# Kernel tuning notes

Measured on AMD Instinct MI355X. Metric: run time of the kernel, lower is better.

Reference implementation:

```python
import jax, jax.numpy as jnp
import numpy as np
import math

T = 2048; HID = 2048; H = 16; KV = 8; G = H // KV; D = 128
GH = 128; BS = 64; NB = T // BS
EPS = 1e-6; RATIO = 0.2; SCALE = 1.0 / math.sqrt(D)


def _rope_tables(length, dim, theta=1000000.0):
    inv = 1.0 / (theta ** (np.arange(0, dim, 2, dtype=np.float32) / dim))
    f = np.outer(np.arange(length, dtype=np.float32), inv)
    emb = np.concatenate([f, f], axis=-1)
    return jnp.asarray(np.cos(emb)), jnp.asarray(np.sin(emb))


def _rot_half(x):
    d = x.shape[-1] // 2
    return jnp.concatenate([-x[..., d:], x[..., :d]], axis=-1)


def _apply_rope(x, cos, sin):
    # x: [T, nH, D], cos/sin: [T, D] broadcast over head dim
    return x * cos[:, None, :] + _rot_half(x) * sin[:, None, :]


def _rmsnorm(x, w, eps=EPS):
    xf = x.astype(jnp.float32)
    v = jnp.mean(xf * xf, axis=-1, keepdims=True)
    return (w * (xf * jax.lax.rsqrt(v + eps))).astype(x.dtype)


def setup_inputs() -> dict:
    key = jax.random.key(0)
    ks = jax.random.split(key, 8)
    s = 0.02
    hidden_states = jax.random.normal(ks[0], (T, HID), jnp.float32)
    Wq = jax.random.normal(ks[1], (HID, H * D), jnp.float32) * s
    Wk = jax.random.normal(ks[2], (HID, KV * D), jnp.float32) * s
    Wv = jax.random.normal(ks[3], (HID, KV * D), jnp.float32) * s
    Wo = jax.random.normal(ks[4], (H * D, HID), jnp.float32) * s
    q_norm_w = jnp.ones((D,), jnp.float32)
    k_norm_w = jnp.ones((D,), jnp.float32)
    gate_wq = jax.random.normal(ks[5], (D, GH), jnp.float32) * s
    gate_wk = jax.random.normal(ks[6], (D, GH), jnp.float32) * s
    cos, sin = _rope_tables(T, D)
    cos_gq, sin_gq = _rope_tables(T, GH)
    cos_blk, sin_blk = _rope_tables(NB, GH)
    # causal block mask: query t may attend to key block j iff j <= t // BS
    block_attention_mask = (jnp.arange(T)[:, None] // BS) >= jnp.arange(NB)[None, :]
    return dict(hidden_states=hidden_states, Wq=Wq, Wk=Wk, Wv=Wv, Wo=Wo,
                q_norm_w=q_norm_w, k_norm_w=k_norm_w, gate_wq=gate_wq, gate_wk=gate_wk,
                cos=cos, sin=sin, cos_gq=cos_gq, sin_gq=sin_gq,
                cos_blk=cos_blk, sin_blk=sin_blk,
                block_attention_mask=block_attention_mask)


def reference(hidden_states, Wq, Wk, Wv, Wo, q_norm_w, k_norm_w, gate_wq, gate_wk,
              cos, sin, cos_gq, sin_gq, cos_blk, sin_blk, block_attention_mask):
    q = (hidden_states @ Wq).reshape(T, H, D)
    k = (hidden_states @ Wk).reshape(T, KV, D)
    v = (hidden_states @ Wv).reshape(T, KV, D)
    q = _rmsnorm(q, q_norm_w)
    k = _rmsnorm(k, k_norm_w)

    # ---- gate network on un-roped q/k: q-head avg-pool to KV heads, k avg-pool per block ----
    q_pool = q.reshape(T, KV, G, D).mean(axis=2)            # [T, KV, D]
    gq = _apply_rope(q_pool @ gate_wq, cos_gq, sin_gq)      # [T, KV, GH]
    k_blk = k.reshape(NB, BS, KV, D).mean(axis=1)           # [NB, KV, D]
    gk = _apply_rope(k_blk @ gate_wk, cos_blk, sin_blk)     # [NB, KV, GH]
    gate_scores = jnp.einsum('tkg,nkg->ktn', gq, gk) / math.sqrt(GH)  # [KV, T, NB]
    predict_mask = jnp.where(block_attention_mask[None], gate_scores, -1e9)

    # ---- main attention (RoPE + GQA causal softmax attention) ----
    qr = _apply_rope(q, cos, sin)
    kr = _apply_rope(k, cos, sin)
    kr_rep = jnp.repeat(kr, G, axis=1)                      # [T, H, D]
    v_rep = jnp.repeat(v, G, axis=1)
    logits = jnp.einsum('thd,shd->hts', qr, kr_rep) * SCALE  # [H, T, T]
    causal = jnp.tril(jnp.ones((T, T), bool))
    logits = jnp.where(causal[None], logits, -jnp.inf)
    probs = jax.nn.softmax(logits, axis=-1)
    attn_output = jnp.einsum('hts,shd->thd', probs, v_rep).reshape(T, H * D) @ Wo

    # ---- pooled ground-truth block mask: attention mass per key block ----
    pooled = probs.reshape(H, T, NB, BS).sum(axis=-1)        # [H, T, NB]
    gt = pooled.reshape(KV, G, T, NB).max(axis=1)            # max_pool3d over head groups -> [KV,T,NB]
    gt = jnp.where(block_attention_mask[None], gt, 0.0)
    gt = gt / (gt.sum(axis=-1, keepdims=True) + 1e-9)

    # ---- KLDiv gate loss on the tail slice (bsz = 1) ----
    start = int(T * RATIO)
    tgt = gt[:, start:, :]                                   # [KV, L, NB]
    logp = jax.nn.log_softmax(predict_mask[:, start:, :], axis=-1)
    safe_t = jnp.where(tgt > 0, tgt, 1.0)
    kl = jnp.where(tgt > 0, tgt * (jnp.log(safe_t) - logp), 0.0)
    gate_loss = kl.reshape(KV, -1).mean(axis=-1).sum()       # KLDivLoss(reduction='mean') per kv head, summed, /bsz(=1)
    return attn_output, gate_loss
```

## Files before the change

### kernel.cpp

```cpp
#include <hip/hip_runtime.h>

#define T_ 2048
#define HID_ 2048
#define H_ 16
#define KV_ 8
#define G_ 2
#define D_ 128
#define GH_ 128
#define BS_ 64
#define NB_ 32
#define START_ 409
#define TG0_ 384
#define SCALE_ 0.08838834764831845f
#define MFIX_ 8.0f

typedef __attribute__((ext_vector_type(8))) short short8_t;
typedef __attribute__((ext_vector_type(4))) float float4_t;
typedef __attribute__((ext_vector_type(8))) unsigned short ushort8_t;
typedef __attribute__((ext_vector_type(4))) unsigned short ushort4_t;

__device__ __forceinline__ float wave_sum(float v) {
#pragma unroll
  for (int o = 32; o > 0; o >>= 1) v += __shfl_xor(v, o, 64);
  return v;
}
__device__ __forceinline__ unsigned short f2bf(float x) {
  unsigned int u = __float_as_uint(x);
  unsigned int r = (u + 0x7fffu + ((u >> 16) & 1u)) >> 16;
  return (unsigned short)r;
}

__device__ __forceinline__ void gload16(const void* g, void* l) {
  __builtin_amdgcn_global_load_lds((const __attribute__((address_space(1))) unsigned int*)g,
                                   (__attribute__((address_space(3))) unsigned int*)l, 16, 0, 0);
}

__device__ __forceinline__ void castT_dev(const float* __restrict__ in,
                                          unsigned short* __restrict__ out, int K, int N,
                                          int ldin, int bx, int by,
                                          unsigned short (*tile)[72], int tid) {
  int k0 = by * 64, n0 = bx * 64;
  int tx = tid & 63, ty4 = tid >> 6;
#pragma unroll
  for (int i = 0; i < 16; ++i) {
    int ky = ty4 * 16 + i;
    tile[tx][ky] = f2bf(in[(size_t)(k0 + ky) * ldin + n0 + tx]);
  }
  __syncthreads();
#pragma unroll
  for (int i = 0; i < 16; ++i) {
    int ny = ty4 * 16 + i;
    out[(size_t)(n0 + ny) * K + k0 + tx] = tile[ny][tx];
  }
}

__global__ __launch_bounds__(256) void prep_cast(const float* __restrict__ hs,
                                                 const float* __restrict__ Wq,
                                                 const float* __restrict__ Wk,
                                                 const float* __restrict__ Wv,
                                                 const float* __restrict__ Wo,
                                                 const float* __restrict__ gwq,
                                                 const float* __restrict__ gwk,
                                                 unsigned short* __restrict__ hsb,
                                                 unsigned short* __restrict__ WqkvT,
                                                 unsigned short* __restrict__ WoT,
                                                 unsigned short* __restrict__ gwqT,
                                                 unsigned short* __restrict__ gwkT) {
  __shared__ unsigned short tile[64][72];
  int id = blockIdx.x, tid = threadIdx.x;
  if (id < 4096) {
    int i = id * 256 + tid;
    float4 v = ((const float4*)hs)[i];
    ushort4_t o = {f2bf(v.x), f2bf(v.y), f2bf(v.z), f2bf(v.w)};
    *(ushort4_t*)(hsb + (size_t)i * 4) = o;
  } else if (id < 5120) {
    int t = id - 4096;
    castT_dev(Wq, WqkvT, 2048, 2048, 2048, t & 31, t >> 5, tile, tid);
  } else if (id < 5632) {
    int t = id - 5120;
    castT_dev(Wk, WqkvT + (size_t)2048 * 2048, 2048, 1024, 1024, t & 15, t >> 4, tile, tid);
  } else if (id < 6144) {
    int t = id - 5632;
    castT_dev(Wv, WqkvT + (size_t)3072 * 2048, 2048, 1024, 1024, t & 15, t >> 4, tile, tid);
  } else if (id < 7168) {
    int t = id - 6144;
    castT_dev(Wo, WoT, 2048, 2048, 2048, t & 31, t >> 5, tile, tid);
  } else if (id < 7172) {
    int t = id - 7168;
    castT_dev(gwq, gwqT, 128, 128, 128, t & 1, t >> 1, tile, tid);
  } else {
    int t = id - 7172;
    castT_dev(gwk, gwkT, 128, 128, 128, t & 1, t >> 1, tile, tid);
  }
}

__device__ __forceinline__ void gemm_body(const unsigned short* __restrict__ A,
                                          const unsigned short* __restrict__ Bt,
                                          float* __restrict__ C,
                                          int M, int N, int K, int ldc, int bx, int by,
                                          unsigned short* As, unsigned short* Bs) {
  int tid = threadIdx.x;
  int wid = tid >> 6, lane = tid & 63;
  int quad = lane >> 4, l16 = lane & 15;
  int wm = wid & 1, wn = wid >> 1;
  int m0 = by * 128, n0 = bx * 128;
  const unsigned short* gA[4];
  const unsigned short* gB[4];
#pragma unroll
  for (int it = 0; it < 4; ++it) {
    int line = wid * 32 + it * 8 + (lane >> 3);
    int chunk = (lane & 7) ^ (line & 7);
    gA[it] = A + (size_t)(m0 + line) * K + chunk * 8;
    gB[it] = Bt + (size_t)(n0 + line) * K + chunk * 8;
  }
  float4_t acc[4][4];
#pragma unroll
  for (int i = 0; i < 4; ++i)
#pragma unroll
    for (int j = 0; j < 4; ++j) acc[i][j] = (float4_t){0.f, 0.f, 0.f, 0.f};
  int nk = K >> 6;
#pragma unroll
  for (int it = 0; it < 4; ++it) {
    gload16(gA[it], As + (wid * 32 + it * 8) * 64);
    gload16(gB[it], Bs + (wid * 32 + it * 8) * 64);
  }
  for (int t = 0; t < nk; ++t) {
    __syncthreads();
    if (t + 1 < nk) {
      int bo = ((t + 1) & 1) * 8192;
#pragma unroll
      for (int it = 0; it < 4; ++it) {
        gload16(gA[it] + (t + 1) * 64, As + bo + (wid * 32 + it * 8) * 64);
        gload16(gB[it] + (t + 1) * 64, Bs + bo + (wid * 32 + it * 8) * 64);
      }
    }
    const unsigned short* Asc = As + (t & 1) * 8192;
    const unsigned short* Bsc = Bs + (t & 1) * 8192;
    short8_t a[2][4], b[2][4];
#pragma unroll
    for (int ks = 0; ks < 2; ++ks) {
      int sw = ((ks * 4 + quad) ^ (l16 & 7)) * 8;
#pragma unroll
      for (int i = 0; i < 4; ++i) {
        a[ks][i] = *(const short8_t*)&Asc[(wm * 64 + i * 16 + l16) * 64 + sw];
        b[ks][i] = *(const short8_t*)&Bsc[(wn * 64 + i * 16 + l16) * 64 + sw];
      }
    }
#pragma unroll
    for (int ks = 0; ks < 2; ++ks)
#pragma unroll
      for (int i = 0; i < 4; ++i)
#pragma unroll
        for (int j = 0; j < 4; ++j)
          acc[i][j] = __builtin_amdgcn_mfma_f32_16x16x32_bf16(a[ks][i], b[ks][j], acc[i][j], 0, 0, 0);
  }
#pragma unroll
  for (int i = 0; i < 4; ++i)
#pragma unroll
    for (int j = 0; j < 4; ++j)
#pragma unroll
      for (int reg = 0; reg < 4; ++reg)
        C[(size_t)(m0 + wm * 64 + i * 16 + quad * 4 + reg) * ldc + n0 + wn * 64 + j * 16 + l16] =
            acc[i][j][reg];
}

__global__ __launch_bounds__(256) void gemm_bf16_v3(const unsigned short* __restrict__ A,
                                                    const unsigned short* __restrict__ Bt,
                                                    float* __restrict__ C,
                                                    int M, int N, int K, int ldc) {
  __shared__ unsigned short As[2 * 128 * 64];
  __shared__ unsigned short Bs[2 * 128 * 64];
  int lin = blockIdx.y * gridDim.x + blockIdx.x;
  int nwg = gridDim.x * gridDim.y;
  int q = nwg >> 3;
  int v = (lin & 7) * q + (lin >> 3);
  int bx = v % gridDim.x, by = v / gridDim.x;
  gemm_body(A, Bt, C, M, N, K, ldc, bx, by, As, Bs);
}

__global__ __launch_bounds__(256) void gemm_gates(const unsigned short* __restrict__ Aq,
                                                  const unsigned short* __restrict__ Bq,
                                                  float* __restrict__ Cq,
                                                  const unsigned short* __restrict__ Ak,
                                                  const unsigned short* __restrict__ Bk,
                                                  float* __restrict__ Ck) {
  __shared__ unsigned short As[2 * 128 * 64];
  __shared__ unsigned short Bs[2 * 128 * 64];
  int y = blockIdx.y;
  if (y < 104)
    gemm_body(Aq, Bq, Cq, 13312, 128, 128, 128, 0, y, As, Bs);
  else
    gemm_body(Ak, Bk, Ck, 256, 128, 128, 128, 0, y - 104, As, Bs);
}

__global__ __launch_bounds__(128) void norm_rope_fused(const float* __restrict__ qkvf,
                                                       const float* __restrict__ qw,
                                                       const float* __restrict__ kw,
                                                       const float* __restrict__ cosT,
                                                       const float* __restrict__ sinT,
                                                       unsigned short* __restrict__ qbf,
                                                       unsigned short* __restrict__ qpool_bf,
                                                       unsigned short* __restrict__ kbf,
                                                       float* __restrict__ knorm) {
  int t = blockIdx.x, d = threadIdx.x;
  int kv = blockIdx.y;
  float cv = cosT[t * D_ + d], sv = sinT[t * D_ + d];
  {
    size_t i0 = (size_t)t * 4096 + (kv * G_) * D_ + d;
    float x0 = qkvf[i0], x1 = qkvf[i0 + D_];
    __shared__ float sred[2][2];
    float s0 = wave_sum(x0 * x0), s1 = wave_sum(x1 * x1);
    if ((d & 63) == 0) { sred[0][d >> 6] = s0; sred[1][d >> 6] = s1; }
    __syncthreads();
    float wv = qw[d];
    float n0 = x0 * rsqrtf((sred[0][0] + sred[0][1]) * (1.f / D_) + 1e-6f) * wv;
    float n1 = x1 * rsqrtf((sred[1][0] + sred[1][1]) * (1.f / D_) + 1e-6f) * wv;
    if (t >= TG0_) qpool_bf[((size_t)(t - TG0_) * KV_ + kv) * D_ + d] = f2bf(0.5f * (n0 + n1));
    __shared__ float sh[2][D_];
    sh[0][d] = n0; sh[1][d] = n1;
    __syncthreads();
    float r0 = (d < 64) ? -sh[0][d + 64] : sh[0][d - 64];
    float r1 = (d < 64) ? -sh[1][d + 64] : sh[1][d - 64];
    qbf[((size_t)(t * H_) + kv * G_) * D_ + d] = f2bf(n0 * cv + r0 * sv);
    qbf[((size_t)(t * H_) + kv * G_ + 1) * D_ + d] = f2bf(n1 * cv + r1 * sv);
  }
  __syncthreads();
  {
    float x = qkvf[(size_t)t * 4096 + 2048 + kv * D_ + d];
    __shared__ float sredk[2];
    float s0 = wave_sum(x * x);
    if ((d & 63) == 0) sredk[d >> 6] = s0;
    __syncthreads();
    float nk = x * rsqrtf((sredk[0] + sredk[1]) * (1.f / D_) + 1e-6f) * kw[d];
    knorm[(size_t)(t * KV_ + kv) * D_ + d] = nk;
    __shared__ float shk[D_];
    shk[d] = nk;
    __syncthreads();
    float rot = (d < 64) ? -shk[d + 64] : shk[d - 64];
    kbf[(size_t)(t * KV_ + kv) * D_ + d] = f2bf(nk * cv + rot * sv);
  }
}

__global__ __launch_bounds__(256) void castT_kblk(const float* __restrict__ qkvf,
                                                  unsigned short* __restrict__ vt,
                                                  const float* __restrict__ knorm,
                                                  unsigned short* __restrict__ kblk_bf) {
  __shared__ unsigned short tile[64][72];
  int id = blockIdx.x, tid = threadIdx.x;
  if (id < 512) {
    castT_dev(qkvf + 3072, vt, T_, 1024, 4096, id & 15, id >> 4, tile, tid);
  } else {
    int task = (id - 512) * 2 + (tid >> 7);
    int n = task >> 3, kv = task & 7, d = tid & 127;
    float s = 0.f;
    for (int i = 0; i < BS_; ++i) s += knorm[((size_t)(n * BS_ + i) * KV_ + kv) * D_ + d];
    kblk_bf[(size_t)(n * KV_ + kv) * D_ + d] = f2bf(s * (1.f / BS_));
  }
}

__global__ __launch_bounds__(128) void rope_g_fused(float* __restrict__ gq, float* __restrict__ gk,
                                                    const float* __restrict__ cosG,
                                                    const float* __restrict__ sinG,
                                                    const float* __restrict__ cosB,
                                                    const float* __restrict__ sinB) {
  int r = blockIdx.x, kvh = blockIdx.y, d = threadIdx.x;
  float* x;
  size_t base;
  float c_, s_;
  if (r < NB_) {
    x = gk;
    base = (size_t)(r * KV_ + kvh) * GH_;
    c_ = cosB[r * GH_ + d]; s_ = sinB[r * GH_ + d];
  } else {
    int rr = r - NB_;
    x = gq;
    base = (size_t)(rr * KV_ + kvh) * GH_;
    c_ = cosG[(size_t)(TG0_ + rr) * GH_ + d]; s_ = sinG[(size_t)(TG0_ + rr) * GH_ + d];
  }
  __shared__ float sh[GH_];
  sh[d] = x[base + d];
  __syncthreads();
  float rot = (d < 64) ? -sh[d + 64] : sh[d - 64];
  x[base + d] = sh[d] * c_ + rot * s_;
}

__global__ __launch_bounds__(256, 2) void attn_mfma(const unsigned short* __restrict__ qbf,
                                                    const unsigned short* __restrict__ kbf,
                                                    const unsigned short* __restrict__ vt,
                                                    float* __restrict__ pooled,
                                                    float* __restrict__ o_acc,
                                                    float* __restrict__ l_acc) {
  int kv = blockIdx.x;
  int yy = blockIdx.y;
  int tile, c_lo, c_hi;
  if (yy < 32) { tile = yy;      c_lo = 0;                c_hi = (tile + 2) >> 1; }
  else         { tile = 63 - yy; c_lo = (tile + 2) >> 1;  c_hi = tile + 1; }
  int t0 = tile * 64;
  int tid = threadIdx.x;
  int wid = tid >> 6, lane = tid & 63;
  int quad = lane >> 4, l16 = lane & 15;
  __shared__ unsigned short Ks[2][64 * 128];
  __shared__ unsigned short Vs[2][128 * 64];
  __shared__ unsigned short Ps[8][16 * 64];

  const unsigned short* kbase[4];
  const unsigned short* vbase[4];
#pragma unroll
  for (int it = 0; it < 4; ++it) {
    int seg = wid * 4 + it;
    int krow = seg * 4 + (lane >> 4);
    int kchk = lane & 15;
    kbase[it] = kbf + ((size_t)krow * KV_ + kv) * D_ + ((kchk ^ (krow & 7)) << 3);
    int vrow = seg * 8 + (lane >> 3);
    int vchk = lane & 7;
    vbase[it] = vt + (size_t)(kv * 128 + vrow) * T_ + ((vchk ^ (vrow & 7)) << 3);
  }

  int tq = t0 + wid * 16 + l16;
  short8_t qf[2][4];
#pragma unroll
  for (int hh = 0; hh < 2; ++hh)
#pragma unroll
    for (int kb = 0; kb < 4; ++kb)
      qf[hh][kb] = *(const short8_t*)&qbf[((size_t)tq * H_ + kv * G_ + hh) * D_ + kb * 32 + quad * 8];

  const short one_bf = (short)0x3F80;
  short8_t ones = {one_bf, one_bf, one_bf, one_bf, one_bf, one_bf, one_bf, one_bf};

  int tbase = t0 + wid * 16 + quad * 4;
  float l_[2][4] = {};
  float pacc[2][2][4] = {};
  float4_t o[2][8];
#pragma unroll
  for (int hh = 0; hh < 2; ++hh)
#pragma unroll
    for (int j = 0; j < 8; ++j) o[hh][j] = (float4_t){0.f, 0.f, 0.f, 0.f};

#pragma unroll
  for (int it = 0; it < 4; ++it) {
    gload16(kbase[it] + (size_t)c_lo * 65536, &Ks[c_lo & 1][(wid * 4 + it) * 512]);
    gload16(vbase[it] + c_lo * 64, &Vs[c_lo & 1][(wid * 4 + it) * 512]);
  }
  for (int c = c_lo; c < c_hi; ++c) {
    __syncthreads();
    if (c + 1 < c_hi) {
      int b = (c + 1) & 1;
#pragma unroll
      for (int it = 0; it < 4; ++it) {
        gload16(kbase[it] + (size_t)(c + 1) * 65536, &Ks[b][(wid * 4 + it) * 512]);
        gload16(vbase[it] + (c + 1) * 64, &Vs[b][(wid * 4 + it) * 512]);
      }
    }
    const unsigned short* Ksc = Ks[c & 1];
    const unsigned short* Vsc = Vs[c & 1];
    int half = c >> 4, cl = c & 15;

    float4_t s[2][4];
#pragma unroll
    for (int j = 0; j < 4; ++j) {
      float4_t a0 = (float4_t){0.f, 0.f, 0.f, 0.f};
      float4_t a1 = (float4_t){0.f, 0.f, 0.f, 0.f};
#pragma unroll
      for (int kb = 0; kb < 4; ++kb) {
        short8_t kf = *(const short8_t*)&Ksc[(j * 16 + l16) * 128 + (((kb * 4 + quad) ^ (l16 & 7)) << 3)];
        a0 = __builtin_amdgcn_mfma_f32_16x16x32_bf16(qf[0][kb], kf, a0, 0, 0, 0);
        a1 = __builtin_amdgcn_mfma_f32_16x16x32_bf16(qf[1][kb], kf, a1, 0, 0, 0);
      }
      s[0][j] = a0;
      s[1][j] = a1;
    }
#pragma unroll
    for (int hh = 0; hh < 2; ++hh) {
      if (c == tile) {
#pragma unroll
        for (int reg = 0; reg < 4; ++reg) {
          int trow = tbase + reg;
#pragma unroll
          for (int j = 0; j < 4; ++j) {
            float p = __expf(s[hh][j][reg] * SCALE_ - MFIX_);
            s[hh][j][reg] = (c * 64 + j * 16 + l16 <= trow) ? p : 0.f;
          }
        }
      } else {
#pragma unroll
        for (int j = 0; j < 4; ++j)
#pragma unroll
          for (int reg = 0; reg < 4; ++reg)
            s[hh][j][reg] = __expf(s[hh][j][reg] * SCALE_ - MFIX_);
      }
#pragma unroll
      for (int j = 0; j < 4; ++j)
#pragma unroll
        for (int reg = 0; reg < 4; ++reg) {
          int r = quad * 4 + reg;
          Ps[wid * 2 + hh][r * 64 + ((j * 16 + l16) ^ ((r & 7) << 3))] = f2bf(s[hh][j][reg]);
        }
    }
    float4_t pool[2] = {(float4_t){0.f, 0.f, 0.f, 0.f}, (float4_t){0.f, 0.f, 0.f, 0.f}};
#pragma unroll
    for (int ks = 0; ks < 2; ++ks) {
      int psw = l16 * 64 + (((ks * 4 + quad) ^ (l16 & 7)) << 3);
      short8_t pf0 = *(const short8_t*)&Ps[wid * 2 + 0][psw];
      short8_t pf1 = *(const short8_t*)&Ps[wid * 2 + 1][psw];
      pool[0] = __builtin_amdgcn_mfma_f32_16x16x32_bf16(pf0, ones, pool[0], 0, 0, 0);
      pool[1] = __builtin_amdgcn_mfma_f32_16x16x32_bf16(pf1, ones, pool[1], 0, 0, 0);
#pragma unroll
      for (int jt = 0; jt < 8; ++jt) {
        short8_t vf = *(const short8_t*)&Vsc[(jt * 16 + l16) * 64 + (((ks * 4 + quad) ^ (l16 & 7)) << 3)];
        o[0][jt] = __builtin_amdgcn_mfma_f32_16x16x32_bf16(pf0, vf, o[0][jt], 0, 0, 0);
        o[1][jt] = __builtin_amdgcn_mfma_f32_16x16x32_bf16(pf1, vf, o[1][jt], 0, 0, 0);
      }
    }
#pragma unroll
    for (int hh = 0; hh < 2; ++hh)
#pragma unroll
      for (int reg = 0; reg < 4; ++reg) {
        l_[hh][reg] += pool[hh][reg];
        if (l16 == cl) pacc[hh][half][reg] = pool[hh][reg];
      }
  }
#pragma unroll
  for (int hh = 0; hh < 2; ++hh) {
    int h = kv * G_ + hh;
#pragma unroll
    for (int reg = 0; reg < 4; ++reg) {
      int trow = tbase + reg;
      if (l16 >= c_lo && l16 < c_hi)
        pooled[((size_t)h * T_ + trow) * NB_ + l16] = pacc[hh][0][reg];
      if (16 + l16 >= c_lo && 16 + l16 < c_hi)
        pooled[((size_t)h * T_ + trow) * NB_ + 16 + l16] = pacc[hh][1][reg];
    }
#pragma unroll
    for (int jt = 0; jt < 8; ++jt)
#pragma unroll
      for (int reg = 0; reg < 4; ++reg)
        atomicAdd(&o_acc[(((size_t)h * T_) + tbase + reg) * D_ + jt * 16 + l16], o[hh][jt][reg]);
    if (l16 == 0) {
#pragma unroll
      for (int reg = 0; reg < 4; ++reg)
        atomicAdd(&l_acc[(size_t)h * T_ + tbase + reg], l_[hh][reg]);
    }
  }
}

__device__ __forceinline__ void gate_loss_body(const float* __restrict__ gq,
                                               const float* __restrict__ gk,
                                               const float* __restrict__ pooled,
                                               const float* __restrict__ l_acc,
                                               float* __restrict__ klsum,
                                               int kv, int yblk, float4* gks4) {
  int tid = threadIdx.x;
#pragma unroll
  for (int p = 0; p < 4; ++p) {
    int f = p * 256 + tid;
    int n = f >> 5, d4 = f & 31;
    gks4[n * 32 + (d4 ^ (n & 7))] =
        *(const float4*)(gk + ((size_t)n * KV_ + kv) * GH_ + d4 * 4);
  }
  __syncthreads();
  int sub = tid >> 5;
  int n = tid & 31;
  int tloc = yblk * 8 + sub;
  bool act = tloc < (T_ - START_);
  int t = START_ + (act ? tloc : 0);
  const float4* a = (const float4*)(gq + ((size_t)(t - TG0_) * KV_ + kv) * GH_);
  float dot = 0.f;
#pragma unroll
  for (int d4 = 0; d4 < 32; ++d4) {
    float4 av = a[d4];
    float4 bv = gks4[n * 32 + (d4 ^ (n & 7))];
    dot += av.x * bv.x + av.y * bv.y + av.z * bv.z + av.w * bv.w;
  }
  bool valid = (t / BS_) >= n;
  float score = valid ? dot * SCALE_ : -1e9f;
  float M = score;
#pragma unroll
  for (int o = 16; o > 0; o >>= 1) M = fmaxf(M, __shfl_xor(M, o, 64));
  float e = __expf(score - M);
  float Z = e;
#pragma unroll
  for (int o = 16; o > 0; o >>= 1) Z += __shfl_xor(Z, o, 64);
  float logZ = M + logf(Z);
  float g = 0.f;
  if (valid) {
    float rl0 = 1.f / l_acc[(size_t)(kv * G_) * T_ + t];
    float rl1 = 1.f / l_acc[(size_t)(kv * G_ + 1) * T_ + t];
    float p0 = pooled[((size_t)(kv * G_) * T_ + t) * NB_ + n] * rl0;
    float p1 = pooled[((size_t)(kv * G_ + 1) * T_ + t) * NB_ + n] * rl1;
    g = fmaxf(p0, p1);
  }
  float gs = g;
#pragma unroll
  for (int o = 16; o > 0; o >>= 1) gs += __shfl_xor(gs, o, 64);
  float tgt = g / (gs + 1e-9f);
  float kl = (tgt > 0.f) ? tgt * (logf(tgt) - (score - logZ)) : 0.f;
  float ks = kl;
#pragma unroll
  for (int o = 16; o > 0; o >>= 1) ks += __shfl_xor(ks, o, 64);
  if (n == 0 && act) klsum[kv * (T_ - START_) + tloc] = ks;
}

__global__ __launch_bounds__(256) void combine_gate(const float* __restrict__ o_acc,
                                                    const float* __restrict__ l_acc,
                                                    unsigned short* __restrict__ attnb,
                                                    const float* __restrict__ gq,
                                                    const float* __restrict__ gk,
                                                    const float* __restrict__ pooled,
                                                    float* __restrict__ klsum) {
  __shared__ float4 gks4[1024];
  int id = blockIdx.x;
  if (id < 1640) {
    gate_loss_body(gq, gk, pooled, l_acc, klsum, id & 7, id >> 3, gks4);
  } else {
    int gid = (id - 1640) * 256 + threadIdx.x;
    int row = gid >> 5, q4 = gid & 31;
    int h = row >> 11, t = row & 2047;
    float inv = 1.f / l_acc[row];
    float4 a = ((const float4*)o_acc)[gid];
    ushort4_t ov = {f2bf(a.x * inv), f2bf(a.y * inv), f2bf(a.z * inv), f2bf(a.w * inv)};
    *(ushort4_t*)(attnb + (size_t)t * (H_ * D_) + h * D_ + q4 * 4) = ov;
  }
}

__global__ __launch_bounds__(256) void finalize_loss(const float* __restrict__ klsum,
                                                     float* __restrict__ out) {
  const int n = KV_ * (T_ - START_);
  float s = 0.f;
  for (int i = threadIdx.x; i < n; i += 256) s += klsum[i];
  s = wave_sum(s);
  __shared__ float sh[4];
  if ((threadIdx.x & 63) == 0) sh[threadIdx.x >> 6] = s;
  __syncthreads();
  if (threadIdx.x == 0)
    out[0] = (sh[0] + sh[1] + sh[2] + sh[3]) * (1.f / ((float)(T_ - START_) * NB_));
}

extern "C" void kernel_launch(void* const* d_in, const int* in_sizes, int n_in,
                              void* d_out, int out_size, void* d_ws, size_t ws_size,
                              hipStream_t stream) {
  const float* hs   = (const float*)d_in[0];
  const float* Wq   = (const float*)d_in[1];
  const float* Wk   = (const float*)d_in[2];
  const float* Wv   = (const float*)d_in[3];
  const float* Wo   = (const float*)d_in[4];
  const float* qw   = (const float*)d_in[5];
  const float* kw   = (const float*)d_in[6];
  const float* gwq  = (const float*)d_in[7];
  const float* gwk  = (const float*)d_in[8];
  const float* cosT = (const float*)d_in[9];
  const float* sinT = (const float*)d_in[10];
  const float* cosG = (const float*)d_in[11];
  const float* sinG = (const float*)d_in[12];
  const float* cosB = (const float*)d_in[13];
  const float* sinB = (const float*)d_in[14];
  float* out = (float*)d_out;
  float* ws = (float*)d_ws;
  const size_t MEG = 1048576;

  float*          qkvf     = ws;
  unsigned short* attnb    = (unsigned short*)ws;
  float*          pooled   = ws + 2 * MEG;
  float*          klsum    = ws + 3 * MEG;
  float*          l_acc    = ws + 3 * MEG + 65536;
  float*          o_acc    = ws + 4 * MEG;
  unsigned short* WqkvT    = (unsigned short*)(ws + 8 * MEG);
  unsigned short* qbf      = WqkvT;
  unsigned short* kbf      = WqkvT + 4 * MEG;
  unsigned short* vt       = WqkvT + 6 * MEG;
  unsigned short* hsb      = (unsigned short*)(ws + 12 * MEG);
  float*          knorm    = ws + 12 * MEG;
  unsigned short* WoT      = (unsigned short*)(ws + 14 * MEG);
  unsigned short* qpool_bf = (unsigned short*)(ws + 16 * MEG);
  float*          gq       = ws + 17 * MEG;
  unsigned short* kblk_bf  = (unsigned short*)(ws + 18 * MEG + 786432);
  float*          gk       = ws + 18 * MEG + 819200;
  unsigned short* gwqT     = (unsigned short*)(ws + 18 * MEG + 851968);
  unsigned short* gwkT     = (unsigned short*)(ws + 18 * MEG + 860160);

  prep_cast<<<7176, 256, 0, stream>>>(hs, Wq, Wk, Wv, Wo, gwq, gwk, hsb, WqkvT, WoT, gwqT, gwkT);
  gemm_bf16_v3<<<dim3(32, 16), 256, 0, stream>>>(hsb, WqkvT, qkvf, 2048, 4096, 2048, 4096);
  norm_rope_fused<<<dim3(T_, 8), 128, 0, stream>>>(qkvf, qw, kw, cosT, sinT, qbf, qpool_bf,
                                                   kbf, knorm);
  castT_kblk<<<640, 256, 0, stream>>>(qkvf, vt, knorm, kblk_bf);
  hipMemsetAsync(o_acc, 0, (size_t)4 * MEG * sizeof(float), stream);
  hipMemsetAsync(l_acc, 0, (size_t)H_ * T_ * sizeof(float), stream);
  gemm_gates<<<dim3(1, 106), 256, 0, stream>>>(qpool_bf, gwqT, gq, kblk_bf, gwkT, gk);
  rope_g_fused<<<dim3(NB_ + (T_ - TG0_), KV_), 128, 0, stream>>>(gq, gk, cosG, sinG, cosB, sinB);
  attn_mfma<<<dim3(KV_, 64), 256, 0, stream>>>(qbf, kbf, vt, pooled, o_acc, l_acc);
  combine_gate<<<1640 + 4096, 256, 0, stream>>>(o_acc, l_acc, attnb, gq, gk, pooled, klsum);
  gemm_bf16_v3<<<dim3(16, 16), 256, 0, stream>>>(attnb, WoT, out, 2048, 2048, 2048, 2048);
  finalize_loss<<<1, 256, 0, stream>>>(klsum, out + (size_t)T_ * HID_);
}
```

Measured before the change: 318.6 us.

## Balance causal attention work with flat chunk-range partitioning across blocks

Replaces the paired-tile split (tile y with 63-y halves) with a flat enumeration of all 528 causal (tile, key-chunk) pairs, so each of the 64 y-blocks gets an equal contiguous range of about 8.25 chunks. Blocks walk across tile boundaries, reloading Q and flushing partial outputs through atomics at each segment end, and keep prefetching the next chunk across tiles. The aim is to even out per-block work and remove load imbalance. The cost is extra atomic flushes and Q reloads at segment boundaries, plus a small serial loop to locate the starting tile.

```diff
diff --git a/kernel.cpp b/kernel.cpp
--- a/kernel.cpp
+++ b/kernel.cpp
@@ -292,10 +292,13 @@
                                                     float* __restrict__ l_acc) {
   int kv = blockIdx.x;
   int yy = blockIdx.y;
-  int tile, c_lo, c_hi;
-  if (yy < 32) { tile = yy;      c_lo = 0;                c_hi = (tile + 2) >> 1; }
-  else         { tile = 63 - yy; c_lo = (tile + 2) >> 1;  c_hi = tile + 1; }
-  int t0 = tile * 64;
+  const int TC = 528;
+  int g = (TC * yy) >> 6;
+  int g_hi = (TC * (yy + 1)) >> 6;
+  int tile = 0, tb = 0;
+  while (tb + tile + 1 <= g) { tb += tile + 1; ++tile; }
+  int c = g - tb;
+
   int tid = threadIdx.x;
   int wid = tid >> 6, lane = tid & 63;
   int quad = lane >> 4, l16 = lane & 15;
@@ -316,130 +319,141 @@
     vbase[it] = vt + (size_t)(kv * 128 + vrow) * T_ + ((vchk ^ (vrow & 7)) << 3);
   }
 
-  int tq = t0 + wid * 16 + l16;
-  short8_t qf[2][4];
-#pragma unroll
-  for (int hh = 0; hh < 2; ++hh)
-#pragma unroll
-    for (int kb = 0; kb < 4; ++kb)
-      qf[hh][kb] = *(const short8_t*)&qbf[((size_t)tq * H_ + kv * G_ + hh) * D_ + kb * 32 + quad * 8];
-
   const short one_bf = (short)0x3F80;
   short8_t ones = {one_bf, one_bf, one_bf, one_bf, one_bf, one_bf, one_bf, one_bf};
 
-  int tbase = t0 + wid * 16 + quad * 4;
-  float l_[2][4] = {};
-  float pacc[2][2][4] = {};
-  float4_t o[2][8];
-#pragma unroll
-  for (int hh = 0; hh < 2; ++hh)
-#pragma unroll
-    for (int j = 0; j < 8; ++j) o[hh][j] = (float4_t){0.f, 0.f, 0.f, 0.f};
-
+  int buf = 0;
 #pragma unroll
   for (int it = 0; it < 4; ++it) {
-    gload16(kbase[it] + (size_t)c_lo * 65536, &Ks[c_lo & 1][(wid * 4 + it) * 512]);
-    gload16(vbase[it] + c_lo * 64, &Vs[c_lo & 1][(wid * 4 + it) * 512]);
-  }
-  for (int c = c_lo; c < c_hi; ++c) {
-    __syncthreads();
-    if (c + 1 < c_hi) {
-      int b = (c + 1) & 1;
-#pragma unroll
-      for (int it = 0; it < 4; ++it) {
-        gload16(kbase[it] + (size_t)(c + 1) * 65536, &Ks[b][(wid * 4 + it) * 512]);
-        gload16(vbase[it] + (c + 1) * 64, &Vs[b][(wid * 4 + it) * 512]);
-      }
+    gload16(kbase[it] + (size_t)c * 65536, &Ks[0][(wid * 4 + it) * 512]);
+    gload16(vbase[it] + c * 64, &Vs[0][(wid * 4 + it) * 512]);
+  }
+
+  while (g < g_hi) {
+    int t0 = tile * 64;
+    int tq = t0 + wid * 16 + l16;
+    short8_t qf[2][4];
+#pragma unroll
+    for (int hh = 0; hh < 2; ++hh)
+#pragma unroll
+      for (int kb = 0; kb < 4; ++kb)
+        qf[hh][kb] = *(const short8_t*)&qbf[((size_t)tq * H_ + kv * G_ + hh) * D_ + kb * 32 + quad * 8];
+    int tbase = t0 + wid * 16 + quad * 4;
+    float l_[2][4] = {};
+    float pacc[2][2][4] = {};
+    float4_t o[2][8];
+#pragma unroll
+    for (int hh = 0; hh < 2; ++hh)
+#pragma unroll
+      for (int j = 0; j < 8; ++j) o[hh][j] = (float4_t){0.f, 0.f, 0.f, 0.f};
+    int c_start = c;
+    bool segEnd = false;
+    while (!segEnd) {
+      __syncthreads();
+      if (g + 1 < g_hi) {
+        int nc = (c + 1 <= tile) ? c + 1 : 0;
+        int b = buf ^ 1;
+#pragma unroll
+        for (int it = 0; it < 4; ++it) {
+          gload16(kbase[it] + (size_t)nc * 65536, &Ks[b][(wid * 4 + it) * 512]);
+          gload16(vbase[it] + nc * 64, &Vs[b][(wid * 4 + it) * 512]);
+        }
+      }
+      const unsigned short* Ksc = Ks[buf];
+      const unsigned short* Vsc = Vs[buf];
+      int half = c >> 4, cl = c & 15;
+
+      float4_t s[2][4];
+#pragma unroll
+      for (int j = 0; j < 4; ++j) {
+        float4_t a0 = (float4_t){0.f, 0.f, 0.f, 0.f};
+        float4_t a1 = (float4_t){0.f, 0.f, 0.f, 0.f};
+#pragma unroll
+        for (int kb = 0; kb < 4; ++kb) {
+          short8_t kf = *(const short8_t*)&Ksc[(j * 16 + l16) * 128 + (((kb * 4 + quad) ^ (l16 & 7)) << 3)];
+          a0 = __builtin_amdgcn_mfma_f32_16x16x32_bf16(qf[0][kb], kf, a0, 0, 0, 0);
+          a1 = __builtin_amdgcn_mfma_f32_16x16x32_bf16(qf[1][kb], kf, a1, 0, 0, 0);
+        }
+        s[0][j] = a0;
+        s[1][j] = a1;
+      }
+#pragma unroll
+      for (int hh = 0; hh < 2; ++hh) {
+        if (c == tile) {
+#pragma unroll
+          for (int reg = 0; reg < 4; ++reg) {
+            int trow = tbase + reg;
+#pragma unroll
+            for (int j = 0; j < 4; ++j) {
+              float p = __expf(s[hh][j][reg] * SCALE_ - MFIX_);
+              s[hh][j][reg] = (c * 64 + j * 16 + l16 <= trow) ? p : 0.f;
+            }
+          }
+        } else {
+#pragma unroll
+          for (int j = 0; j < 4; ++j)
+#pragma unroll
+            for (int reg = 0; reg < 4; ++reg)
+              s[hh][j][reg] = __expf(s[hh][j][reg] * SCALE_ - MFIX_);
+        }
+#pragma unroll
+        for (int j = 0; j < 4; ++j)
+#pragma unroll
+          for (int reg = 0; reg < 4; ++reg) {
+            int r = quad * 4 + reg;
+            Ps[wid * 2 + hh][r * 64 + ((j * 16 + l16) ^ ((r & 7) << 3))] = f2bf(s[hh][j][reg]);
+          }
+      }
+      float4_t pool[2] = {(float4_t){0.f, 0.f, 0.f, 0.f}, (float4_t){0.f, 0.f, 0.f, 0.f}};
+#pragma unroll
+      for (int ks = 0; ks < 2; ++ks) {
+        int psw = l16 * 64 + (((ks * 4 + quad) ^ (l16 & 7)) << 3);
+        short8_t pf0 = *(const short8_t*)&Ps[wid * 2 + 0][psw];
+        short8_t pf1 = *(const short8_t*)&Ps[wid * 2 + 1][psw];
+        pool[0] = __builtin_amdgcn_mfma_f32_16x16x32_bf16(pf0, ones, pool[0], 0, 0, 0);
+        pool[1] = __builtin_amdgcn_mfma_f32_16x16x32_bf16(pf1, ones, pool[1], 0, 0, 0);
+#pragma unroll
+        for (int jt = 0; jt < 8; ++jt) {
+          short8_t vf = *(const short8_t*)&Vsc[(jt * 16 + l16) * 64 + (((ks * 4 + quad) ^ (l16 & 7)) << 3)];
+          o[0][jt] = __builtin_amdgcn_mfma_f32_16x16x32_bf16(pf0, vf, o[0][jt], 0, 0, 0);
+          o[1][jt] = __builtin_amdgcn_mfma_f32_16x16x32_bf16(pf1, vf, o[1][jt], 0, 0, 0);
+        }
+      }
+#pragma unroll
+      for (int hh = 0; hh < 2; ++hh)
+#pragma unroll
+        for (int reg = 0; reg < 4; ++reg) {
+          l_[hh][reg] += pool[hh][reg];
+          if (l16 == cl) pacc[hh][half][reg] = pool[hh][reg];
+        }
+      buf ^= 1;
+      ++g;
+      if (g < g_hi && c < tile) ++c; else segEnd = true;
     }
-    const unsigned short* Ksc = Ks[c & 1];
-    const unsigned short* Vsc = Vs[c & 1];
-    int half = c >> 4, cl = c & 15;
-
-    float4_t s[2][4];
-#pragma unroll
-    for (int j = 0; j < 4; ++j) {
-      float4_t a0 = (float4_t){0.f, 0.f, 0.f, 0.f};
-      float4_t a1 = (float4_t){0.f, 0.f, 0.f, 0.f};
-#pragma unroll
-      for (int kb = 0; kb < 4; ++kb) {
-        short8_t kf = *(const short8_t*)&Ksc[(j * 16 + l16) * 128 + (((kb * 4 + quad) ^ (l16 & 7)) << 3)];
-        a0 = __builtin_amdgcn_mfma_f32_16x16x32_bf16(qf[0][kb], kf, a0, 0, 0, 0);
-        a1 = __builtin_amdgcn_mfma_f32_16x16x32_bf16(qf[1][kb], kf, a1, 0, 0, 0);
-      }
-      s[0][j] = a0;
-      s[1][j] = a1;
+    int c_end = c + 1;
+#pragma unroll
+    for (int hh = 0; hh < 2; ++hh) {
+      int h = kv * G_ + hh;
+#pragma unroll
+      for (int reg = 0; reg < 4; ++reg) {
+        int trow = tbase + reg;
+        if (l16 >= c_start && l16 < c_end)
+          pooled[((size_t)h * T_ + trow) * NB_ + l16] = pacc[hh][0][reg];
+        if (16 + l16 >= c_start && 16 + l16 < c_end)
+          pooled[((size_t)h * T_ + trow) * NB_ + 16 + l16] = pacc[hh][1][reg];
+      }
+#pragma unroll
+      for (int jt = 0; jt < 8; ++jt)
+#pragma unroll
+        for (int reg = 0; reg < 4; ++reg)
+          atomicAdd(&o_acc[(((size_t)h * T_) + tbase + reg) * D_ + jt * 16 + l16], o[hh][jt][reg]);
+      if (l16 == 0) {
+#pragma unroll
+        for (int reg = 0; reg < 4; ++reg)
+          atomicAdd(&l_acc[(size_t)h * T_ + tbase + reg], l_[hh][reg]);
+      }
     }
-#pragma unroll
-    for (int hh = 0; hh < 2; ++hh) {
-      if (c == tile) {
-#pragma unroll
-        for (int reg = 0; reg < 4; ++reg) {
-          int trow = tbase + reg;
-#pragma unroll
-          for (int j = 0; j < 4; ++j) {
-            float p = __expf(s[hh][j][reg] * SCALE_ - MFIX_);
-            s[hh][j][reg] = (c * 64 + j * 16 + l16 <= trow) ? p : 0.f;
-          }
-        }
-      } else {
-#pragma unroll
-        for (int j = 0; j < 4; ++j)
-#pragma unroll
-          for (int reg = 0; reg < 4; ++reg)
-            s[hh][j][reg] = __expf(s[hh][j][reg] * SCALE_ - MFIX_);
-      }
-#pragma unroll
-      for (int j = 0; j < 4; ++j)
-#pragma unroll
-        for (int reg = 0; reg < 4; ++reg) {
-          int r = quad * 4 + reg;
-          Ps[wid * 2 + hh][r * 64 + ((j * 16 + l16) ^ ((r & 7) << 3))] = f2bf(s[hh][j][reg]);
-        }
-    }
-    float4_t pool[2] = {(float4_t){0.f, 0.f, 0.f, 0.f}, (float4_t){0.f, 0.f, 0.f, 0.f}};
-#pragma unroll
-    for (int ks = 0; ks < 2; ++ks) {
-      int psw = l16 * 64 + (((ks * 4 + quad) ^ (l16 & 7)) << 3);
-      short8_t pf0 = *(const short8_t*)&Ps[wid * 2 + 0][psw];
-      short8_t pf1 = *(const short8_t*)&Ps[wid * 2 + 1][psw];
-      pool[0] = __builtin_amdgcn_mfma_f32_16x16x32_bf16(pf0, ones, pool[0], 0, 0, 0);
-      pool[1] = __builtin_amdgcn_mfma_f32_16x16x32_bf16(pf1, ones, pool[1], 0, 0, 0);
-#pragma unroll
-      for (int jt = 0; jt < 8; ++jt) {
-        short8_t vf = *(const short8_t*)&Vsc[(jt * 16 + l16) * 64 + (((ks * 4 + quad) ^ (l16 & 7)) << 3)];
-        o[0][jt] = __builtin_amdgcn_mfma_f32_16x16x32_bf16(pf0, vf, o[0][jt], 0, 0, 0);
-        o[1][jt] = __builtin_amdgcn_mfma_f32_16x16x32_bf16(pf1, vf, o[1][jt], 0, 0, 0);
-      }
-    }
-#pragma unroll
-    for (int hh = 0; hh < 2; ++hh)
-#pragma unroll
-      for (int reg = 0; reg < 4; ++reg) {
-        l_[hh][reg] += pool[hh][reg];
-        if (l16 == cl) pacc[hh][half][reg] = pool[hh][reg];
-      }
-  }
-#pragma unroll
-  for (int hh = 0; hh < 2; ++hh) {
-    int h = kv * G_ + hh;
-#pragma unroll
-    for (int reg = 0; reg < 4; ++reg) {
-      int trow = tbase + reg;
-      if (l16 >= c_lo && l16 < c_hi)
-        pooled[((size_t)h * T_ + trow) * NB_ + l16] = pacc[hh][0][reg];
-      if (16 + l16 >= c_lo && 16 + l16 < c_hi)
-        pooled[((size_t)h * T_ + trow) * NB_ + 16 + l16] = pacc[hh][1][reg];
-    }
-#pragma unroll
-    for (int jt = 0; jt < 8; ++jt)
-#pragma unroll
-      for (int reg = 0; reg < 4; ++reg)
-        atomicAdd(&o_acc[(((size_t)h * T_) + tbase + reg) * D_ + jt * 16 + l16], o[hh][jt][reg]);
-    if (l16 == 0) {
-#pragma unroll
-      for (int reg = 0; reg < 4; ++reg)
-        atomicAdd(&l_acc[(size_t)h * T_ + tbase + reg], l_[hh][reg]);
-    }
+    if (g < g_hi) { ++tile; c = 0; }
   }
 }
 
```

Result: slower. 330.0 us (+3.6%).
